# Kernel tuning notes

Hardware: AMD Instinct MI355X
Metric: run time of the kernel (lower is better)

## Reference

```python
import jax, jax.numpy as jnp
import numpy as np

CP_SIZE = 2
CP_RANK = 0
SLIDING_WINDOW = 1024
S_GLOBAL = 4096
T_LOCAL = S_GLOBAL // CP_SIZE
NQ, NK, HN = 16, 8, 128


def setup_inputs() -> dict:
    key = jax.random.key(0)
    kq, kk, kv = jax.random.split(key, 3)
    return {
        # local zigzag-sliced queries on this cp rank: [t_local, nq, hn]
        "query": jax.random.normal(kq, (T_LOCAL, NQ, HN), dtype=jnp.float32),
        # K/V AFTER all-gather across cp ranks (rank-chunk concatenated layout,
        # exactly what gather_from_sequence_parallel_region produces): [S, nk, hn]
        "key": jax.random.normal(kk, (S_GLOBAL, NK, HN), dtype=jnp.float32),
        "value": jax.random.normal(kv, (S_GLOBAL, NK, HN), dtype=jnp.float32),
        # global packed-seq boundaries (single sub-sequence)
        "cu_seqlens": jnp.array([0, S_GLOBAL], dtype=jnp.int32),
    }


def _zigzag_perm(seq_len_global: int, cp: int) -> jnp.ndarray:
    """global position g -> offset into the rank-gathered K/V tensor."""
    cs = seq_len_global // (2 * cp)
    g = jnp.arange(seq_len_global)
    q_idx = g // cs
    owner = jnp.where(q_idx < cp, q_idx, 2 * cp - 1 - q_idx)
    local_in_rank = jnp.where(q_idx < cp, g - owner * cs,
                              cs + (g - (2 * cp - 1 - owner) * cs))
    return owner * (2 * cs) + local_in_rank


def _zigzag_rows(local_len: int, rank: int, cp: int) -> jnp.ndarray:
    """global positions of this rank's local Q tokens (zigzag layout)."""
    cs = local_len // 2
    first = jnp.arange(rank * cs, (rank + 1) * cs)
    second = jnp.arange((2 * cp - rank - 1) * cs, (2 * cp - rank) * cs)
    return jnp.concatenate([first, second])


def reference(query, key, value, cu_seqlens):
    S = key.shape[0]
    t_local, nq, hn = query.shape
    nk = key.shape[1]
    scale = hn ** (-0.5)

    # un-permute gathered K/V from rank-chunk zigzag layout to global order
    perm = _zigzag_perm(S, CP_SIZE)
    k_full = key[perm]    # [S, nk, hn]
    v_full = value[perm]

    # GQA: replicate kv heads to match q heads (enable_gqa)
    rep = nq // nk
    k_full = jnp.repeat(k_full, rep, axis=1)  # [S, nq, hn]
    v_full = jnp.repeat(v_full, rep, axis=1)

    # causal + sliding-window mask from zigzag global row indices
    row = _zigzag_rows(t_local, CP_RANK, CP_SIZE)  # [t_local]
    col = jnp.arange(S)
    forbid = col[None, :] > row[:, None]
    if SLIDING_WINDOW is not None and SLIDING_WINDOW > 0:
        forbid = forbid | (col[None, :] < row[:, None] - (SLIDING_WINDOW - 1))
    bias = jnp.where(forbid, jnp.finfo(query.dtype).min, 0.0).astype(query.dtype)

    # SDPA: scores [nq, t_local, S]
    scores = jnp.einsum('shd,thd->hst', query, k_full) * scale + bias[None]
    probs = jax.nn.softmax(scores, axis=-1)
    out = jnp.einsum('hst,thd->shd', probs, v_full)  # [t_local, nq, hn]
    return out.reshape(t_local, nq * hn)
```

## Files before the change

### kernel.cpp

```cpp
#include <hip/hip_runtime.h>
#include <hip/hip_bf16.h>

#define T_LOCAL 2048
#define S_GLOBAL 4096
#define NQ 16
#define NK 8
#define HN 128

#define SCALE2 0.12753102541996022f

typedef __attribute__((ext_vector_type(8))) short short8;
typedef __attribute__((ext_vector_type(4))) float f32x4;

static __device__ __forceinline__ ushort f2bf(float x) {
  unsigned u = __builtin_bit_cast(unsigned, x);
  unsigned r = (u + 0x7fffu + ((u >> 16) & 1u)) >> 16;
  return (ushort)r;
}

static __device__ __forceinline__ void gload16(const ushort* g, ushort* lds) {
  __builtin_amdgcn_global_load_lds(
      (const __attribute__((address_space(1))) void*)g,
      (__attribute__((address_space(3))) void*)lds, 16, 0, 0);
}

__global__ void k_convert(const float* __restrict__ K, ushort* __restrict__ Kb) {
  size_t i = ((size_t)blockIdx.x * 256 + threadIdx.x) * 4;
  float4 v = *(const float4*)(K + i);
  ushort4 o;
  o.x = f2bf(v.x); o.y = f2bf(v.y); o.z = f2bf(v.z); o.w = f2bf(v.w);
  *(ushort4*)(Kb + i) = o;
}

__global__ void v_transpose(const float* __restrict__ V, ushort* __restrict__ Vt) {
  int bid = blockIdx.x;
  int h  = bid >> 7;
  int r  = bid & 127;
  int d0 = (r >> 6) << 6;
  int p0 = (r & 63) << 6;
  __shared__ ushort tile[64][72];
  int tx = threadIdx.x & 15, ty = threadIdx.x >> 4;
  #pragma unroll
  for (int it = 0; it < 4; ++it) {
    int p = p0 + it * 16 + ty;
    int d = tx * 4;
    float4 v = *(const float4*)(V + ((size_t)p * NK + h) * HN + d0 + d);
    tile[d + 0][it * 16 + ty] = f2bf(v.x);
    tile[d + 1][it * 16 + ty] = f2bf(v.y);
    tile[d + 2][it * 16 + ty] = f2bf(v.z);
    tile[d + 3][it * 16 + ty] = f2bf(v.w);
  }
  __syncthreads();
  #pragma unroll
  for (int it = 0; it < 4; ++it) {
    int d  = it * 16 + ty;
    int pb = tx * 4;
    ushort4 o;
    o.x = tile[d][pb + 0]; o.y = tile[d][pb + 1];
    o.z = tile[d][pb + 2]; o.w = tile[d][pb + 3];
    *(ushort4*)(Vt + ((size_t)h * HN + d0 + d) * S_GLOBAL + p0 + pb) = o;
  }
}

__global__ __launch_bounds__(256, 4)
void attn_kernel(const float* __restrict__ Q, const ushort* __restrict__ Kb,
                 const ushort* __restrict__ Vt, float* __restrict__ Out) {
  __shared__ ushort Klds[2][64 * 128];
  __shared__ ushort Vlds[2][128 * 64];
  __shared__ ushort Pl[4][16][56];

  const int lane = threadIdx.x & 63;
  const int w    = threadIdx.x >> 6;
  const int qcol = lane & 15;
  const int g    = lane >> 4;

  const int bid  = blockIdx.x;
  const int kvh  = bid & 7;
  const int j    = bid >> 3;
  const int head = 2 * kvh + (j & 1);
  const int slot = j >> 1;
  const int Tt   = (slot & 1) ? 16 + (slot >> 1) : (slot >> 1);
  const int tb   = Tt << 6;
  const int tw   = tb + w * 16;
  const int tq   = tw + qcol;

  int c0, nC, a0 = 0, n;
  if (tb < 1024) { c0 = 0; nC = Tt + 1; n = nC; }
  else { c0 = 16; nC = Tt - 15; a0 = Tt + 32; n = nC + (32 - Tt); }

  short8 qf[4];
  {
    const float* qb = Q + ((size_t)tq * NQ + head) * HN;
    #pragma unroll
    for (int ds = 0; ds < 4; ++ds) {
      const float4* p4 = (const float4*)(qb + ds * 32 + g * 8);
      float4 a = p4[0], b = p4[1];
      short8 f;
      f[0] = f2bf(a.x); f[1] = f2bf(a.y); f[2] = f2bf(a.z); f[3] = f2bf(a.w);
      f[4] = f2bf(b.x); f[5] = f2bf(b.y); f[6] = f2bf(b.z); f[7] = f2bf(b.w);
      qf[ds] = f;
    }
  }
  asm volatile("s_waitcnt vmcnt(0)" ::: "memory");

  f32x4 acc[8];
  #pragma unroll
  for (int i = 0; i < 8; ++i) acc[i] = (f32x4){0.f, 0.f, 0.f, 0.f};
  float m_run = -1e30f, l_run = 0.f;

  ushort* prow = &Pl[w][qcol][0];
  const int rx = (qcol & 7) << 4;

  auto chunk_p0 = [&](int i) {
    return ((i < nC) ? (c0 + i) : (a0 + (i - nC))) << 6;
  };

  auto stage = [&](int b, int p0) {
    #pragma unroll
    for (int t = 0; t < 4; ++t) {
      int idx = (w * 4 + t) * 64 + lane;
      int row = idx >> 4;
      int cu  = (idx & 15) ^ (row & 7);
      gload16(Kb + ((size_t)(p0 + row) * NK + kvh) * HN + cu * 8,
              &Klds[b][(w * 4 + t) * 512]);
    }
    #pragma unroll
    for (int t = 0; t < 4; ++t) {
      int idx = (w * 4 + t) * 64 + lane;
      int d   = idx >> 3;
      int pu  = (idx & 7) ^ ((idx >> 3) & 7);
      gload16(Vt + ((size_t)kvh * HN + d) * S_GLOBAL + p0 + pu * 8,
              &Vlds[b][(w * 4 + t) * 512]);
    }
  };

  stage(0, chunk_p0(0));

  for (int c = 0; c < n; ++c) {
    if (c + 1 < n) {
      stage((c + 1) & 1, chunk_p0(c + 1));
      asm volatile("s_waitcnt vmcnt(8)" ::: "memory");
    } else {
      asm volatile("s_waitcnt vmcnt(0)" ::: "memory");
    }
    __builtin_amdgcn_s_barrier();

    const int p0   = chunk_p0(c);
    const bool anti = p0 >= 2048;
    const char* Klc = (const char*)Klds[c & 1];
    const char* Vlc = (const char*)Vlds[c & 1];

    #pragma unroll
    for (int psub = 0; psub < 2; ++psub) {
      const int p0s = p0 + psub * 32;
      const bool activ = anti ? (p0s + 31 >= tw + 2049) : (p0s <= tw + 15);
      if (activ) {
        const bool needmask = anti ? (p0s < tw + 2064) : (p0s + 31 > tw);

        short8 kf[2][4];
        #pragma unroll
        for (int sub = 0; sub < 2; ++sub) {
          const int rbase = (psub * 32 + sub * 16 + qcol) * 256;
          #pragma unroll
          for (int ds = 0; ds < 4; ++ds)
            kf[sub][ds] = *(const short8*)(Klc + rbase + ((ds * 64 + g * 16) ^ rx));
        }

        f32x4 st[2];
        st[0] = (f32x4){0.f, 0.f, 0.f, 0.f};
        st[1] = (f32x4){0.f, 0.f, 0.f, 0.f};
        #pragma unroll
        for (int sub = 0; sub < 2; ++sub)
          #pragma unroll
          for (int ds = 0; ds < 4; ++ds)
            st[sub] = __builtin_amdgcn_mfma_f32_16x16x32_bf16(kf[sub][ds], qf[ds], st[sub], 0, 0, 0);

        float s_[8];
        #pragma unroll
        for (int sub = 0; sub < 2; ++sub) {
          #pragma unroll
          for (int r = 0; r < 4; ++r) {
            float sv = st[sub][r] * SCALE2;
            if (needmask) {
              int p = p0s + sub * 16 + g * 4 + r;
              bool ok = anti ? (p >= tq + 2049) : (p <= tq);
              sv = ok ? sv : -INFINITY;
            }
            s_[sub * 4 + r] = sv;
          }
        }

        float mt = s_[0];
        #pragma unroll
        for (int i = 1; i < 8; ++i) mt = fmaxf(mt, s_[i]);
        mt = fmaxf(mt, __shfl_xor(mt, 16));
        mt = fmaxf(mt, __shfl_xor(mt, 32));
        float mnew = fmaxf(m_run, mt);
        float fsc  = __builtin_amdgcn_exp2f(m_run - mnew);
        float pv[8];
        float ps = 0.f;
        #pragma unroll
        for (int i = 0; i < 8; ++i) { pv[i] = __builtin_amdgcn_exp2f(s_[i] - mnew); ps += pv[i]; }
        ps += __shfl_xor(ps, 16);
        ps += __shfl_xor(ps, 32);
        l_run = l_run * fsc + ps;
        m_run = mnew;
        #pragma unroll
        for (int i = 0; i < 8; ++i) acc[i] *= fsc;

        unsigned lo0 = (unsigned)f2bf(pv[0]) | ((unsigned)f2bf(pv[1]) << 16);
        unsigned hi0 = (unsigned)f2bf(pv[2]) | ((unsigned)f2bf(pv[3]) << 16);
        unsigned lo1 = (unsigned)f2bf(pv[4]) | ((unsigned)f2bf(pv[5]) << 16);
        unsigned hi1 = (unsigned)f2bf(pv[6]) | ((unsigned)f2bf(pv[7]) << 16);
        *(uint2*)(prow + g * 4)      = make_uint2(lo0, hi0);
        *(uint2*)(prow + 16 + g * 4) = make_uint2(lo1, hi1);
        short8 pf = *(const short8*)(prow + g * 8);

        short8 vf[8];
        #pragma unroll
        for (int db = 0; db < 8; ++db)
          vf[db] = *(const short8*)(Vlc + (db * 16 + qcol) * 128 + ((psub * 64 + g * 16) ^ rx));

        #pragma unroll
        for (int db = 0; db < 8; ++db)
          acc[db] = __builtin_amdgcn_mfma_f32_16x16x32_bf16(vf[db], pf, acc[db], 0, 0, 0);
      }
    }
    __builtin_amdgcn_s_barrier();
  }

  float inv = 1.0f / l_run;
  float* ob = Out + (size_t)tq * (NQ * HN) + head * HN + g * 4;
  #pragma unroll
  for (int db = 0; db < 8; ++db) {
    float4 o;
    o.x = acc[db][0] * inv; o.y = acc[db][1] * inv;
    o.z = acc[db][2] * inv; o.w = acc[db][3] * inv;
    *(float4*)(ob + db * 16) = o;
  }
}

extern "C" void kernel_launch(void* const* d_in, const int* in_sizes, int n_in,
                              void* d_out, int out_size, void* d_ws, size_t ws_size,
                              hipStream_t stream) {
  const float* Q = (const float*)d_in[0];
  const float* K = (const float*)d_in[1];
  const float* V = (const float*)d_in[2];
  float* Out = (float*)d_out;

  ushort* Kb = (ushort*)d_ws;
  ushort* Vt = Kb + (size_t)S_GLOBAL * NK * HN;

  k_convert<<<dim3((S_GLOBAL * NK * HN) / (256 * 4)), dim3(256), 0, stream>>>(K, Kb);
  v_transpose<<<dim3(NK * 2 * (S_GLOBAL / 64)), dim3(256), 0, stream>>>(V, Vt);
  attn_kernel<<<dim3(512), dim3(256), 0, stream>>>(Q, Kb, Vt, Out);
}
```

Before: 146.8 us.

## Split each KV chunk across two wave groups and merge softmax states

Doubles the block to 8 waves. Each group of four query waves now handles one 32-key half of every 64-key chunk, instead of one wave walking both halves in sequence. The two partial online-softmax states (m, l, acc) are merged through LDS at the end. The aim is more waves in flight per block and shorter per-wave serial MFMA chains, to hide latency better. The cost is a final LDS reduction, extra registers, and possible occupancy limits from the 512-thread launch bounds.

```diff
diff --git a/kernel.cpp b/kernel.cpp
--- a/kernel.cpp
+++ b/kernel.cpp
@@ -62,15 +62,17 @@
   }
 }
 
-__global__ __launch_bounds__(256, 4)
+__global__ __launch_bounds__(512, 4)
 void attn_kernel(const float* __restrict__ Q, const ushort* __restrict__ Kb,
                  const ushort* __restrict__ Vt, float* __restrict__ Out) {
   __shared__ ushort Klds[2][64 * 128];
   __shared__ ushort Vlds[2][128 * 64];
-  __shared__ ushort Pl[4][16][56];
+  __shared__ ushort Pl[8][16][56];
 
   const int lane = threadIdx.x & 63;
   const int w    = threadIdx.x >> 6;
+  const int qg   = w & 3;
+  const int ks   = w >> 2;
   const int qcol = lane & 15;
   const int g    = lane >> 4;
 
@@ -81,7 +83,7 @@
   const int slot = j >> 1;
   const int Tt   = (slot & 1) ? 16 + (slot >> 1) : (slot >> 1);
   const int tb   = Tt << 6;
-  const int tw   = tb + w * 16;
+  const int tw   = tb + qg * 16;
   const int tq   = tw + qcol;
 
   int c0, nC, a0 = 0, n;
@@ -117,20 +119,20 @@
 
   auto stage = [&](int b, int p0) {
     #pragma unroll
-    for (int t = 0; t < 4; ++t) {
-      int idx = (w * 4 + t) * 64 + lane;
+    for (int t = 0; t < 2; ++t) {
+      int idx = (w * 2 + t) * 64 + lane;
       int row = idx >> 4;
       int cu  = (idx & 15) ^ (row & 7);
       gload16(Kb + ((size_t)(p0 + row) * NK + kvh) * HN + cu * 8,
-              &Klds[b][(w * 4 + t) * 512]);
-    }
-    #pragma unroll
-    for (int t = 0; t < 4; ++t) {
-      int idx = (w * 4 + t) * 64 + lane;
+              &Klds[b][(w * 2 + t) * 512]);
+    }
+    #pragma unroll
+    for (int t = 0; t < 2; ++t) {
+      int idx = (w * 2 + t) * 64 + lane;
       int d   = idx >> 3;
-      int pu  = (idx & 7) ^ ((idx >> 3) & 7);
+      int pu  = (idx & 7) ^ (d & 7);
       gload16(Vt + ((size_t)kvh * HN + d) * S_GLOBAL + p0 + pu * 8,
-              &Vlds[b][(w * 4 + t) * 512]);
+              &Vlds[b][(w * 2 + t) * 512]);
     }
   };
 
@@ -139,7 +141,7 @@
   for (int c = 0; c < n; ++c) {
     if (c + 1 < n) {
       stage((c + 1) & 1, chunk_p0(c + 1));
-      asm volatile("s_waitcnt vmcnt(8)" ::: "memory");
+      asm volatile("s_waitcnt vmcnt(4)" ::: "memory");
     } else {
       asm volatile("s_waitcnt vmcnt(0)" ::: "memory");
     }
@@ -150,93 +152,112 @@
     const char* Klc = (const char*)Klds[c & 1];
     const char* Vlc = (const char*)Vlds[c & 1];
 
-    #pragma unroll
-    for (int psub = 0; psub < 2; ++psub) {
-      const int p0s = p0 + psub * 32;
-      const bool activ = anti ? (p0s + 31 >= tw + 2049) : (p0s <= tw + 15);
-      if (activ) {
-        const bool needmask = anti ? (p0s < tw + 2064) : (p0s + 31 > tw);
-
-        short8 kf[2][4];
+    const int p0s = p0 + ks * 32;
+    const bool activ = anti ? (p0s + 31 >= tw + 2049) : (p0s <= tw + 15);
+    if (activ) {
+      const bool needmask = anti ? (p0s < tw + 2064) : (p0s + 31 > tw);
+
+      short8 kf[2][4];
+      #pragma unroll
+      for (int sub = 0; sub < 2; ++sub) {
+        const int rbase = (ks * 32 + sub * 16 + qcol) * 256;
         #pragma unroll
-        for (int sub = 0; sub < 2; ++sub) {
-          const int rbase = (psub * 32 + sub * 16 + qcol) * 256;
-          #pragma unroll
-          for (int ds = 0; ds < 4; ++ds)
-            kf[sub][ds] = *(const short8*)(Klc + rbase + ((ds * 64 + g * 16) ^ rx));
+        for (int ds = 0; ds < 4; ++ds)
+          kf[sub][ds] = *(const short8*)(Klc + rbase + ((ds * 64 + g * 16) ^ rx));
+      }
+      short8 vf[8];
+      #pragma unroll
+      for (int db = 0; db < 8; ++db)
+        vf[db] = *(const short8*)(Vlc + (db * 16 + qcol) * 128 + ((ks * 64 + g * 16) ^ rx));
+
+      f32x4 st[2];
+      st[0] = (f32x4){0.f, 0.f, 0.f, 0.f};
+      st[1] = (f32x4){0.f, 0.f, 0.f, 0.f};
+      #pragma unroll
+      for (int sub = 0; sub < 2; ++sub)
+        #pragma unroll
+        for (int ds = 0; ds < 4; ++ds)
+          st[sub] = __builtin_amdgcn_mfma_f32_16x16x32_bf16(kf[sub][ds], qf[ds], st[sub], 0, 0, 0);
+
+      float s_[8];
+      #pragma unroll
+      for (int sub = 0; sub < 2; ++sub) {
+        #pragma unroll
+        for (int r = 0; r < 4; ++r) {
+          float sv = st[sub][r] * SCALE2;
+          if (needmask) {
+            int p = p0s + sub * 16 + g * 4 + r;
+            bool ok = anti ? (p >= tq + 2049) : (p <= tq);
+            sv = ok ? sv : -INFINITY;
+          }
+          s_[sub * 4 + r] = sv;
         }
-
-        f32x4 st[2];
-        st[0] = (f32x4){0.f, 0.f, 0.f, 0.f};
-        st[1] = (f32x4){0.f, 0.f, 0.f, 0.f};
-        #pragma unroll
-        for (int sub = 0; sub < 2; ++sub)
-          #pragma unroll
-          for (int ds = 0; ds < 4; ++ds)
-            st[sub] = __builtin_amdgcn_mfma_f32_16x16x32_bf16(kf[sub][ds], qf[ds], st[sub], 0, 0, 0);
-
-        float s_[8];
-        #pragma unroll
-        for (int sub = 0; sub < 2; ++sub) {
-          #pragma unroll
-          for (int r = 0; r < 4; ++r) {
-            float sv = st[sub][r] * SCALE2;
-            if (needmask) {
-              int p = p0s + sub * 16 + g * 4 + r;
-              bool ok = anti ? (p >= tq + 2049) : (p <= tq);
-              sv = ok ? sv : -INFINITY;
-            }
-            s_[sub * 4 + r] = sv;
-          }
-        }
-
-        float mt = s_[0];
-        #pragma unroll
-        for (int i = 1; i < 8; ++i) mt = fmaxf(mt, s_[i]);
-        mt = fmaxf(mt, __shfl_xor(mt, 16));
-        mt = fmaxf(mt, __shfl_xor(mt, 32));
-        float mnew = fmaxf(m_run, mt);
-        float fsc  = __builtin_amdgcn_exp2f(m_run - mnew);
-        float pv[8];
-        float ps = 0.f;
-        #pragma unroll
-        for (int i = 0; i < 8; ++i) { pv[i] = __builtin_amdgcn_exp2f(s_[i] - mnew); ps += pv[i]; }
-        ps += __shfl_xor(ps, 16);
-        ps += __shfl_xor(ps, 32);
-        l_run = l_run * fsc + ps;
-        m_run = mnew;
-        #pragma unroll
-        for (int i = 0; i < 8; ++i) acc[i] *= fsc;
-
-        unsigned lo0 = (unsigned)f2bf(pv[0]) | ((unsigned)f2bf(pv[1]) << 16);
-        unsigned hi0 = (unsigned)f2bf(pv[2]) | ((unsigned)f2bf(pv[3]) << 16);
-        unsigned lo1 = (unsigned)f2bf(pv[4]) | ((unsigned)f2bf(pv[5]) << 16);
-        unsigned hi1 = (unsigned)f2bf(pv[6]) | ((unsigned)f2bf(pv[7]) << 16);
-        *(uint2*)(prow + g * 4)      = make_uint2(lo0, hi0);
-        *(uint2*)(prow + 16 + g * 4) = make_uint2(lo1, hi1);
-        short8 pf = *(const short8*)(prow + g * 8);
-
-        short8 vf[8];
-        #pragma unroll
-        for (int db = 0; db < 8; ++db)
-          vf[db] = *(const short8*)(Vlc + (db * 16 + qcol) * 128 + ((psub * 64 + g * 16) ^ rx));
-
-        #pragma unroll
-        for (int db = 0; db < 8; ++db)
-          acc[db] = __builtin_amdgcn_mfma_f32_16x16x32_bf16(vf[db], pf, acc[db], 0, 0, 0);
       }
+
+      float mt = s_[0];
+      #pragma unroll
+      for (int i = 1; i < 8; ++i) mt = fmaxf(mt, s_[i]);
+      mt = fmaxf(mt, __shfl_xor(mt, 16));
+      mt = fmaxf(mt, __shfl_xor(mt, 32));
+      float mnew = fmaxf(m_run, mt);
+      float fsc  = __builtin_amdgcn_exp2f(m_run - mnew);
+      float pv[8];
+      float ps = 0.f;
+      #pragma unroll
+      for (int i = 0; i < 8; ++i) { pv[i] = __builtin_amdgcn_exp2f(s_[i] - mnew); ps += pv[i]; }
+      ps += __shfl_xor(ps, 16);
+      ps += __shfl_xor(ps, 32);
+      l_run = l_run * fsc + ps;
+      m_run = mnew;
+      #pragma unroll
+      for (int i = 0; i < 8; ++i) acc[i] *= fsc;
+
+      unsigned lo0 = (unsigned)f2bf(pv[0]) | ((unsigned)f2bf(pv[1]) << 16);
+      unsigned hi0 = (unsigned)f2bf(pv[2]) | ((unsigned)f2bf(pv[3]) << 16);
+      unsigned lo1 = (unsigned)f2bf(pv[4]) | ((unsigned)f2bf(pv[5]) << 16);
+      unsigned hi1 = (unsigned)f2bf(pv[6]) | ((unsigned)f2bf(pv[7]) << 16);
+      *(uint2*)(prow + g * 4)      = make_uint2(lo0, hi0);
+      *(uint2*)(prow + 16 + g * 4) = make_uint2(lo1, hi1);
+      short8 pf = *(const short8*)(prow + g * 8);
+
+      #pragma unroll
+      for (int db = 0; db < 8; ++db)
+        acc[db] = __builtin_amdgcn_mfma_f32_16x16x32_bf16(vf[db], pf, acc[db], 0, 0, 0);
     }
     __builtin_amdgcn_s_barrier();
   }
 
-  float inv = 1.0f / l_run;
-  float* ob = Out + (size_t)tq * (NQ * HN) + head * HN + g * 4;
-  #pragma unroll
-  for (int db = 0; db < 8; ++db) {
-    float4 o;
-    o.x = acc[db][0] * inv; o.y = acc[db][1] * inv;
-    o.z = acc[db][2] * inv; o.w = acc[db][3] * inv;
-    *(float4*)(ob + db * 16) = o;
+  __syncthreads();
+  float* mb  = (float*)&Klds[0][0];
+  float* mlb = (float*)&Vlds[0][0];
+  if (ks == 1) {
+    if (g == 0) {
+      mlb[(qg * 16 + qcol) * 2 + 0] = m_run;
+      mlb[(qg * 16 + qcol) * 2 + 1] = l_run;
+    }
+    #pragma unroll
+    for (int db = 0; db < 8; ++db)
+      *(f32x4*)&mb[(qg * 16 + qcol) * 128 + db * 16 + g * 4] = acc[db];
+  }
+  __syncthreads();
+  if (ks == 0) {
+    float mr = mlb[(qg * 16 + qcol) * 2 + 0];
+    float lr = mlb[(qg * 16 + qcol) * 2 + 1];
+    float mnew = fmaxf(m_run, mr);
+    float f0 = __builtin_amdgcn_exp2f(m_run - mnew);
+    float fr = __builtin_amdgcn_exp2f(mr - mnew);
+    float inv = 1.0f / (l_run * f0 + lr * fr);
+    float* ob = Out + (size_t)tq * (NQ * HN) + head * HN + g * 4;
+    #pragma unroll
+    for (int db = 0; db < 8; ++db) {
+      f32x4 o = *(const f32x4*)&mb[(qg * 16 + qcol) * 128 + db * 16 + g * 4];
+      float4 r;
+      r.x = (acc[db][0] * f0 + o[0] * fr) * inv;
+      r.y = (acc[db][1] * f0 + o[1] * fr) * inv;
+      r.z = (acc[db][2] * f0 + o[2] * fr) * inv;
+      r.w = (acc[db][3] * f0 + o[3] * fr) * inv;
+      *(float4*)(ob + db * 16) = r;
+    }
   }
 }
 
@@ -253,5 +274,5 @@
 
   k_convert<<<dim3((S_GLOBAL * NK * HN) / (256 * 4)), dim3(256), 0, stream>>>(K, Kb);
   v_transpose<<<dim3(NK * 2 * (S_GLOBAL / 64)), dim3(256), 0, stream>>>(V, Vt);
-  attn_kernel<<<dim3(512), dim3(256), 0, stream>>>(Q, Kb, Vt, Out);
-}
+  attn_kernel<<<dim3(512), dim3(512), 0, stream>>>(Q, Kb, Vt, Out);
+}
```

After: 140.2 us. 4.5% less time.
